# Kernel optimization log

Measured on AMD Instinct MI355X. Metric: run time of the kernel, lower is better.

## Reference

```python
import jax, jax.numpy as jnp
import numpy as np


def _layernorm(x, g, b, eps=1e-5):
    mu = x.mean(-1, keepdims=True)
    var = ((x - mu) ** 2).mean(-1, keepdims=True)
    return (x - mu) / jnp.sqrt(var + eps) * g + b


def _bilinear_sample(feat, coords):
    # feat: (B,C,H,W,D); coords: (B,C,N,2) normalized to [-1,1]
    # torch.grid_sample(mode='bilinear', padding_mode='zeros', align_corners=True)
    B, C, H, W, D = feat.shape
    x = (coords[..., 0] + 1.0) * 0.5 * (W - 1)  # grid x -> width axis
    y = (coords[..., 1] + 1.0) * 0.5 * (H - 1)  # grid y -> height axis
    x0 = jnp.floor(x)
    y0 = jnp.floor(y)
    wx1 = x - x0
    wy1 = y - y0
    bi = jnp.arange(B)[:, None, None]
    ci = jnp.arange(C)[None, :, None]

    def corner(yi, xi, w):
        inb = (xi >= 0) & (xi < W) & (yi >= 0) & (yi < H)
        xc = jnp.clip(xi, 0, W - 1).astype(jnp.int32)
        yc = jnp.clip(yi, 0, H - 1).astype(jnp.int32)
        v = feat[bi, ci, yc, xc]  # (B,C,N,D) gather
        return v * (w * inb)[..., None]

    return (corner(y0, x0, (1 - wy1) * (1 - wx1))
            + corner(y0, x0 + 1, (1 - wy1) * wx1)
            + corner(y0 + 1, x0, wy1 * (1 - wx1))
            + corner(y0 + 1, x0 + 1, wy1 * wx1))


def setup_inputs() -> dict:
    key = jax.random.key(0)
    ks = jax.random.split(key, 12)
    B, C, N, D, H, W = 2, 8, 16384, 256, 64, 64
    s = 1.0 / np.sqrt(D).astype(np.float32)
    return {
        "queries": jax.random.normal(ks[0], (B, N, D), jnp.float32),
        "image_features": jax.random.normal(ks[1], (B, C, H, W, D), jnp.float32),
        "pixel_coords": jax.random.uniform(ks[2], (B, C, N, 2), jnp.float32) * 2.0 - 1.0,
        "valid_mask": jax.random.randint(ks[3], (B, C, N), 0, 2).astype(jnp.int32),
        "Wq": jax.random.normal(ks[4], (D, D), jnp.float32) * s,
        "bq": jnp.zeros((D,), jnp.float32),
        "Wkv": jax.random.normal(ks[5], (D, 2 * D), jnp.float32) * s,
        "bkv": jnp.zeros((2 * D,), jnp.float32),
        "Wo": jax.random.normal(ks[6], (D, D), jnp.float32) * s,
        "bo": jnp.zeros((D,), jnp.float32),
        "gamma": jnp.ones((D,), jnp.float32),
        "beta": jnp.zeros((D,), jnp.float32),
    }


def reference(queries, image_features, pixel_coords, valid_mask,
              Wq, bq, Wkv, bkv, Wo, bo, gamma, beta):
    B, N, D = queries.shape
    residual = queries
    qn = _layernorm(queries, gamma, beta)
    sampled = _bilinear_sample(image_features, pixel_coords)      # (B,C,N,D)
    sampled = jnp.transpose(sampled, (0, 2, 1, 3))                 # (B,N,C,D)
    q = qn @ Wq + bq                                               # (B,N,D)
    kv = sampled @ Wkv + bkv                                       # (B,N,C,2D)
    k, v = kv[..., :D], kv[..., D:]
    scores = jnp.einsum('bnd,bncd->bnc', q, k) / jnp.sqrt(jnp.float32(D))
    valid = jnp.transpose(valid_mask, (0, 2, 1)) != 0              # (B,N,C)
    scores = jnp.where(valid, scores, -jnp.inf)
    attn = jax.nn.softmax(scores, axis=-1)
    attn = jnp.where(jnp.isnan(attn), 0.0, attn)                   # all-invalid -> 0
    out = jnp.einsum('bnc,bncd->bnd', attn, v)
    return residual + out @ Wo + bo
```

## Files before the change

### kernel.cpp

```cpp
#include <hip/hip_runtime.h>
#include <math.h>

#define NROWS 32768

typedef __attribute__((ext_vector_type(8))) short short8;
typedef __attribute__((ext_vector_type(4))) float f32x4;

#define WS_ABF    0
#define WS_WVOBF  32768
#define WS_PB     65536
#define WS_BVO    65792
#define WS_FEATBF 8487424

__device__ __forceinline__ unsigned short f2bf(float f) {
    unsigned u = __builtin_bit_cast(unsigned, f);
    u += 0x7FFFu + ((u >> 16) & 1u);
    return (unsigned short)(u >> 16);
}
__device__ __forceinline__ float bf_lo(unsigned u) {
    return __builtin_bit_cast(float, u << 16);
}
__device__ __forceinline__ float bf_hi(unsigned u) {
    return __builtin_bit_cast(float, u & 0xFFFF0000u);
}

__global__ __launch_bounds__(256)
void precompute_kernel(const float* __restrict__ Wq, const float* __restrict__ bq,
                       const float* __restrict__ Wkv, const float* __restrict__ bkv,
                       const float* __restrict__ Wo, const float* __restrict__ feat,
                       float* __restrict__ ws) {
    int t = threadIdx.x;
    int blk = blockIdx.x;
    if (blk >= 514) {
        long i = (long)(blk - 514) * 1024 + t * 4;
        float4 v = *(const float4*)(feat + i);
        unsigned lo = (unsigned)f2bf(v.x) | ((unsigned)f2bf(v.y) << 16);
        unsigned hi = (unsigned)f2bf(v.z) | ((unsigned)f2bf(v.w) << 16);
        *(uint2*)((unsigned short*)(ws + WS_FEATBF) + i) = make_uint2(lo, hi);
        return;
    }
    if (blk < 256) {
        int f = blk;
        const float4* wq4 = (const float4*)(Wq + f * 256);
        const float4* wk4 = (const float4*)(Wkv + (long)t * 512);
        float acc = 0.f;
        #pragma unroll 8
        for (int d4 = 0; d4 < 64; ++d4) {
            float4 a = wq4[d4], b = wk4[d4];
            acc += a.x * b.x + a.y * b.y + a.z * b.z + a.w * b.w;
        }
        ((unsigned short*)(ws + WS_ABF))[t * 256 + f] = f2bf(acc);
    } else if (blk < 512) {
        int e = blk - 256;
        float acc = 0.f;
        for (int g = 0; g < 256; ++g)
            acc = fmaf(Wkv[(long)e * 512 + 256 + g], Wo[g * 256 + t], acc);
        ((unsigned short*)(ws + WS_WVOBF))[t * 256 + e] = f2bf(acc);
    } else if (blk == 512) {
        float acc = 0.f;
        for (int d = 0; d < 256; ++d)
            acc = fmaf(bq[d], Wkv[(long)t * 512 + d], acc);
        ws[WS_PB + t] = acc;
    } else {
        float acc = 0.f;
        for (int g = 0; g < 256; ++g)
            acc = fmaf(bkv[256 + g], Wo[g * 256 + t], acc);
        ws[WS_BVO + t] = acc;
    }
}

#define RPB  32
#define SLOT 260

__global__ __launch_bounds__(256, 4)
void fused_rowpipe(const float* __restrict__ queries, const float* __restrict__ gamma,
                   const float* __restrict__ beta, const float* __restrict__ coords,
                   const int* __restrict__ vmask, const float* __restrict__ bo,
                   const float* __restrict__ ws, float* __restrict__ out) {
    __shared__ float buf[RPB * SLOT + RPB];
    float* ssu = buf + RPB * SLOT;

    const unsigned short* Abf    = (const unsigned short*)(ws + WS_ABF);
    const unsigned short* Wvobf  = (const unsigned short*)(ws + WS_WVOBF);
    const float*          pb     = ws + WS_PB;
    const float*          bvo    = ws + WS_BVO;
    const unsigned short* featbf = (const unsigned short*)(ws + WS_FEATBF);

    int tid = threadIdx.x, wave = tid >> 6, lane = tid & 63;
    long row0 = (long)blockIdx.x * RPB;

    {
        float4 g4 = *(const float4*)(gamma + 4 * lane);
        float4 b4 = *(const float4*)(beta + 4 * lane);
        #pragma unroll
        for (int rr = 0; rr < 8; ++rr) {
            int r = wave * 8 + rr;
            float4 v = *(const float4*)(queries + (row0 + r) * 256 + 4 * lane);
            float s = v.x + v.y + v.z + v.w;
            s += __shfl_xor(s, 32); s += __shfl_xor(s, 16); s += __shfl_xor(s, 8);
            s += __shfl_xor(s, 4);  s += __shfl_xor(s, 2);  s += __shfl_xor(s, 1);
            float mu = s * 0.00390625f;
            float dx = v.x - mu, dy = v.y - mu, dz = v.z - mu, dw = v.w - mu;
            float vv = dx * dx + dy * dy + dz * dz + dw * dw;
            vv += __shfl_xor(vv, 32); vv += __shfl_xor(vv, 16); vv += __shfl_xor(vv, 8);
            vv += __shfl_xor(vv, 4);  vv += __shfl_xor(vv, 2);  vv += __shfl_xor(vv, 1);
            float rstd = rsqrtf(vv * 0.00390625f + 1e-5f);
            float qx = dx * rstd * g4.x + b4.x;
            float qy = dy * rstd * g4.y + b4.y;
            float qz = dz * rstd * g4.z + b4.z;
            float qw = dw * rstd * g4.w + b4.w;
            unsigned lo = (unsigned)f2bf(qx) | ((unsigned)f2bf(qy) << 16);
            unsigned hi = (unsigned)f2bf(qz) | ((unsigned)f2bf(qw) << 16);
            *(uint2*)((unsigned short*)&buf[r * SLOT] + 4 * lane) = make_uint2(lo, hi);
        }
    }
    __syncthreads();

    int r16 = lane & 15, g = lane >> 4;
    f32x4 zero = {0.f, 0.f, 0.f, 0.f};

    {
        f32x4 acc[2][4];
        #pragma unroll
        for (int mt = 0; mt < 2; ++mt)
            #pragma unroll
            for (int nt = 0; nt < 4; ++nt) acc[mt][nt] = zero;

        #pragma unroll
        for (int ks = 0; ks < 8; ++ks) {
            short8 bfr[4], afr[2];
            #pragma unroll
            for (int nt = 0; nt < 4; ++nt)
                bfr[nt] = *(const short8*)(Abf + ((wave * 64 + nt * 16 + r16) << 8) + ks * 32 + g * 8);
            #pragma unroll
            for (int mt = 0; mt < 2; ++mt)
                afr[mt] = *(const short8*)((const unsigned short*)buf + (mt * 16 + r16) * (SLOT * 2) + ks * 32 + g * 8);
            #pragma unroll
            for (int mt = 0; mt < 2; ++mt)
                #pragma unroll
                for (int nt = 0; nt < 4; ++nt)
                    acc[mt][nt] = __builtin_amdgcn_mfma_f32_16x16x32_bf16(afr[mt], bfr[nt], acc[mt][nt], 0, 0, 0);
        }
        __syncthreads();

        float pbv[4];
        #pragma unroll
        for (int nt = 0; nt < 4; ++nt) pbv[nt] = pb[wave * 64 + nt * 16 + r16];
        #pragma unroll
        for (int mt = 0; mt < 2; ++mt)
            #pragma unroll
            for (int nt = 0; nt < 4; ++nt)
                #pragma unroll
                for (int rg = 0; rg < 4; ++rg)
                    buf[(mt * 16 + g * 4 + rg) * SLOT + wave * 64 + nt * 16 + r16] =
                        acc[mt][nt][rg] + pbv[nt];
    }
    __syncthreads();

    for (int rr = 0; rr < 8; ++rr) {
        int r = wave * 8 + rr;
        int rowu = __builtin_amdgcn_readfirstlane((int)(row0 + r));
        int b = rowu >> 14;
        int n = rowu & 16383;

        float4 p4 = *(const float4*)(&buf[r * SLOT + 4 * lane]);

        float4 sc[8];
        float score[8];
        bool vld[8];
        #pragma unroll
        for (int c = 0; c < 8; ++c) {
            long cb = (long)(b * 8 + c) * 16384 + n;
            float cx = coords[2 * cb];
            float cy = coords[2 * cb + 1];
            vld[c] = (vmask[cb] != 0);
            float x = (cx + 1.f) * 31.5f;
            float y = (cy + 1.f) * 31.5f;
            float x0f = floorf(x), y0f = floorf(y);
            float wx = x - x0f, wy = y - y0f;
            int ix0 = (int)x0f, iy0 = (int)y0f;
            int ix1 = ix0 + 1, iy1 = iy0 + 1;
            float bx0 = (ix0 >= 0 && ix0 < 64) ? 1.f : 0.f;
            float bx1 = (ix1 >= 0 && ix1 < 64) ? 1.f : 0.f;
            float by0 = (iy0 >= 0 && iy0 < 64) ? 1.f : 0.f;
            float by1 = (iy1 >= 0 && iy1 < 64) ? 1.f : 0.f;
            int cx0 = min(max(ix0, 0), 63), cx1 = min(max(ix1, 0), 63);
            int cy0 = min(max(iy0, 0), 63), cy1 = min(max(iy1, 0), 63);
            const unsigned short* fb = featbf + ((long)(b * 8 + c) << 20);
            const uint2* r00 = (const uint2*)(fb + ((cy0 * 64 + cx0) << 8)) + lane;
            const uint2* r01 = (const uint2*)(fb + ((cy0 * 64 + cx1) << 8)) + lane;
            const uint2* r10 = (const uint2*)(fb + ((cy1 * 64 + cx0) << 8)) + lane;
            const uint2* r11 = (const uint2*)(fb + ((cy1 * 64 + cx1) << 8)) + lane;
            float w00 = (1.f - wy) * (1.f - wx) * by0 * bx0;
            float w01 = (1.f - wy) * wx * by0 * bx1;
            float w10 = wy * (1.f - wx) * by1 * bx0;
            float w11 = wy * wx * by1 * bx1;
            uint2 v00 = *r00, v01 = *r01, v10 = *r10, v11 = *r11;
            float4 s;
            s.x = w00 * bf_lo(v00.x) + w01 * bf_lo(v01.x) + w10 * bf_lo(v10.x) + w11 * bf_lo(v11.x);
            s.y = w00 * bf_hi(v00.x) + w01 * bf_hi(v01.x) + w10 * bf_hi(v10.x) + w11 * bf_hi(v11.x);
            s.z = w00 * bf_lo(v00.y) + w01 * bf_lo(v01.y) + w10 * bf_lo(v10.y) + w11 * bf_lo(v11.y);
            s.w = w00 * bf_hi(v00.y) + w01 * bf_hi(v01.y) + w10 * bf_hi(v10.y) + w11 * bf_hi(v11.y);
            sc[c] = s;
            float t = s.x * p4.x + s.y * p4.y + s.z * p4.z + s.w * p4.w;
            t += __shfl_xor(t, 32); t += __shfl_xor(t, 16); t += __shfl_xor(t, 8);
            t += __shfl_xor(t, 4);  t += __shfl_xor(t, 2);  t += __shfl_xor(t, 1);
            score[c] = t * 0.0625f;
        }

        float m = -INFINITY;
        #pragma unroll
        for (int c = 0; c < 8; ++c) if (vld[c]) m = fmaxf(m, score[c]);
        float4 sb = {0.f, 0.f, 0.f, 0.f};
        float sa = 0.f;
        if (m > -INFINITY) {
            float w[8], s = 0.f;
            #pragma unroll
            for (int c = 0; c < 8; ++c) { w[c] = vld[c] ? __expf(score[c] - m) : 0.f; s += w[c]; }
            float inv = 1.f / s;
            #pragma unroll
            for (int c = 0; c < 8; ++c) {
                float a = w[c] * inv;
                sb.x = fmaf(a, sc[c].x, sb.x);
                sb.y = fmaf(a, sc[c].y, sb.y);
                sb.z = fmaf(a, sc[c].z, sb.z);
                sb.w = fmaf(a, sc[c].w, sb.w);
            }
            sa = 1.f;
        }
        unsigned lo = (unsigned)f2bf(sb.x) | ((unsigned)f2bf(sb.y) << 16);
        unsigned hi = (unsigned)f2bf(sb.z) | ((unsigned)f2bf(sb.w) << 16);
        *(uint2*)((unsigned short*)&buf[r * SLOT] + 4 * lane) = make_uint2(lo, hi);
        if (lane == 0) ssu[r] = sa;
    }
    __syncthreads();

    {
        f32x4 acc2[2][4];
        #pragma unroll
        for (int mt = 0; mt < 2; ++mt)
            #pragma unroll
            for (int nt = 0; nt < 4; ++nt) acc2[mt][nt] = zero;

        #pragma unroll
        for (int ks = 0; ks < 8; ++ks) {
            short8 bfr[4], afr[2];
            #pragma unroll
            for (int nt = 0; nt < 4; ++nt)
                bfr[nt] = *(const short8*)(Wvobf + ((wave * 64 + nt * 16 + r16) << 8) + ks * 32 + g * 8);
            #pragma unroll
            for (int mt = 0; mt < 2; ++mt)
                afr[mt] = *(const short8*)((const unsigned short*)buf + (mt * 16 + r16) * (SLOT * 2) + ks * 32 + g * 8);
            #pragma unroll
            for (int mt = 0; mt < 2; ++mt)
                #pragma unroll
                for (int nt = 0; nt < 4; ++nt)
                    acc2[mt][nt] = __builtin_amdgcn_mfma_f32_16x16x32_bf16(afr[mt], bfr[nt], acc2[mt][nt], 0, 0, 0);
        }
        __syncthreads();

        #pragma unroll
        for (int mt = 0; mt < 2; ++mt)
            #pragma unroll
            for (int nt = 0; nt < 4; ++nt)
                #pragma unroll
                for (int rg = 0; rg < 4; ++rg)
                    buf[(mt * 16 + g * 4 + rg) * SLOT + wave * 64 + nt * 16 + r16] = acc2[mt][nt][rg];
    }
    __syncthreads();

    {
        float4 bvo4 = *(const float4*)(bvo + 4 * lane);
        float4 bo4  = *(const float4*)(bo + 4 * lane);
        #pragma unroll
        for (int rr = 0; rr < 8; ++rr) {
            int r = wave * 8 + rr;
            float4 q4 = *(const float4*)(queries + (row0 + r) * 256 + 4 * lane);
            float4 a4 = *(const float4*)(&buf[r * SLOT + 4 * lane]);
            float su = ssu[r];
            float4 o;
            o.x = q4.x + a4.x + su * bvo4.x + bo4.x;
            o.y = q4.y + a4.y + su * bvo4.y + bo4.y;
            o.z = q4.z + a4.z + su * bvo4.z + bo4.z;
            o.w = q4.w + a4.w + su * bvo4.w + bo4.w;
            *(float4*)(out + (row0 + r) * 256 + 4 * lane) = o;
        }
    }
}

extern "C" void kernel_launch(void* const* d_in, const int* in_sizes, int n_in,
                              void* d_out, int out_size, void* d_ws, size_t ws_size,
                              hipStream_t stream) {
    const float* queries = (const float*)d_in[0];
    const float* feat    = (const float*)d_in[1];
    const float* coords  = (const float*)d_in[2];
    const int*   vmask   = (const int*)  d_in[3];
    const float* Wq      = (const float*)d_in[4];
    const float* bq      = (const float*)d_in[5];
    const float* Wkv     = (const float*)d_in[6];
    const float* bkv     = (const float*)d_in[7];
    const float* Wo      = (const float*)d_in[8];
    const float* bo      = (const float*)d_in[9];
    const float* gamma   = (const float*)d_in[10];
    const float* beta    = (const float*)d_in[11];
    float* out = (float*)d_out;
    float* ws  = (float*)d_ws;

    precompute_kernel<<<514 + 16384, 256, 0, stream>>>(Wq, bq, Wkv, bkv, Wo, feat, ws);
    fused_rowpipe<<<NROWS / RPB, 256, 0, stream>>>(queries, gamma, beta, coords, vmask, bo, ws, out);
}
```

Baseline: 259.4 us.

## Halve rows per block, use online softmax, stash queries in registers

Cuts rows per block from 32 to 16, so each wave runs one MFMA row tile and the grid has twice as many blocks. The eight-camera softmax becomes an online (running max/sum) accumulation, so the per-camera sampled vectors and scores no longer sit in registers. The residual query values are kept in registers instead of being reloaded from global memory, and the small precompute loops get unroll pragmas. In exchange, each block reloads the weight fragments over half as many rows, and the online softmax adds extra exp calls and rescaling work.

```diff
diff --git a/kernel.cpp b/kernel.cpp
--- a/kernel.cpp
+++ b/kernel.cpp
@@ -53,23 +53,26 @@
     } else if (blk < 512) {
         int e = blk - 256;
         float acc = 0.f;
+        #pragma unroll 8
         for (int g = 0; g < 256; ++g)
             acc = fmaf(Wkv[(long)e * 512 + 256 + g], Wo[g * 256 + t], acc);
         ((unsigned short*)(ws + WS_WVOBF))[t * 256 + e] = f2bf(acc);
     } else if (blk == 512) {
         float acc = 0.f;
+        #pragma unroll 8
         for (int d = 0; d < 256; ++d)
             acc = fmaf(bq[d], Wkv[(long)t * 512 + d], acc);
         ws[WS_PB + t] = acc;
     } else {
         float acc = 0.f;
+        #pragma unroll 8
         for (int g = 0; g < 256; ++g)
             acc = fmaf(bkv[256 + g], Wo[g * 256 + t], acc);
         ws[WS_BVO + t] = acc;
     }
 }
 
-#define RPB  32
+#define RPB  16
 #define SLOT 260
 
 __global__ __launch_bounds__(256, 4)
@@ -89,13 +92,16 @@
     int tid = threadIdx.x, wave = tid >> 6, lane = tid & 63;
     long row0 = (long)blockIdx.x * RPB;
 
+    float4 qstash[4];
+
     {
         float4 g4 = *(const float4*)(gamma + 4 * lane);
         float4 b4 = *(const float4*)(beta + 4 * lane);
         #pragma unroll
-        for (int rr = 0; rr < 8; ++rr) {
-            int r = wave * 8 + rr;
+        for (int rr = 0; rr < 4; ++rr) {
+            int r = wave * 4 + rr;
             float4 v = *(const float4*)(queries + (row0 + r) * 256 + 4 * lane);
+            qstash[rr] = v;
             float s = v.x + v.y + v.z + v.w;
             s += __shfl_xor(s, 32); s += __shfl_xor(s, 16); s += __shfl_xor(s, 8);
             s += __shfl_xor(s, 4);  s += __shfl_xor(s, 2);  s += __shfl_xor(s, 1);
@@ -120,26 +126,20 @@
     f32x4 zero = {0.f, 0.f, 0.f, 0.f};
 
     {
-        f32x4 acc[2][4];
-        #pragma unroll
-        for (int mt = 0; mt < 2; ++mt)
-            #pragma unroll
-            for (int nt = 0; nt < 4; ++nt) acc[mt][nt] = zero;
+        f32x4 acc[4];
+        #pragma unroll
+        for (int nt = 0; nt < 4; ++nt) acc[nt] = zero;
 
         #pragma unroll
         for (int ks = 0; ks < 8; ++ks) {
-            short8 bfr[4], afr[2];
+            short8 bfr[4], afr;
             #pragma unroll
             for (int nt = 0; nt < 4; ++nt)
                 bfr[nt] = *(const short8*)(Abf + ((wave * 64 + nt * 16 + r16) << 8) + ks * 32 + g * 8);
-            #pragma unroll
-            for (int mt = 0; mt < 2; ++mt)
-                afr[mt] = *(const short8*)((const unsigned short*)buf + (mt * 16 + r16) * (SLOT * 2) + ks * 32 + g * 8);
-            #pragma unroll
-            for (int mt = 0; mt < 2; ++mt)
-                #pragma unroll
-                for (int nt = 0; nt < 4; ++nt)
-                    acc[mt][nt] = __builtin_amdgcn_mfma_f32_16x16x32_bf16(afr[mt], bfr[nt], acc[mt][nt], 0, 0, 0);
+            afr = *(const short8*)((const unsigned short*)buf + r16 * (SLOT * 2) + ks * 32 + g * 8);
+            #pragma unroll
+            for (int nt = 0; nt < 4; ++nt)
+                acc[nt] = __builtin_amdgcn_mfma_f32_16x16x32_bf16(afr, bfr[nt], acc[nt], 0, 0, 0);
         }
         __syncthreads();
 
@@ -147,33 +147,30 @@
         #pragma unroll
         for (int nt = 0; nt < 4; ++nt) pbv[nt] = pb[wave * 64 + nt * 16 + r16];
         #pragma unroll
-        for (int mt = 0; mt < 2; ++mt)
-            #pragma unroll
-            for (int nt = 0; nt < 4; ++nt)
-                #pragma unroll
-                for (int rg = 0; rg < 4; ++rg)
-                    buf[(mt * 16 + g * 4 + rg) * SLOT + wave * 64 + nt * 16 + r16] =
-                        acc[mt][nt][rg] + pbv[nt];
+        for (int nt = 0; nt < 4; ++nt)
+            #pragma unroll
+            for (int rg = 0; rg < 4; ++rg)
+                buf[(g * 4 + rg) * SLOT + wave * 64 + nt * 16 + r16] = acc[nt][rg] + pbv[nt];
     }
     __syncthreads();
 
-    for (int rr = 0; rr < 8; ++rr) {
-        int r = wave * 8 + rr;
+    for (int rr = 0; rr < 4; ++rr) {
+        int r = wave * 4 + rr;
         int rowu = __builtin_amdgcn_readfirstlane((int)(row0 + r));
         int b = rowu >> 14;
         int n = rowu & 16383;
 
         float4 p4 = *(const float4*)(&buf[r * SLOT + 4 * lane]);
 
-        float4 sc[8];
-        float score[8];
-        bool vld[8];
+        float m = -INFINITY, ssum = 0.f;
+        float4 sbacc = {0.f, 0.f, 0.f, 0.f};
+
         #pragma unroll
         for (int c = 0; c < 8; ++c) {
             long cb = (long)(b * 8 + c) * 16384 + n;
             float cx = coords[2 * cb];
             float cy = coords[2 * cb + 1];
-            vld[c] = (vmask[cb] != 0);
+            bool vld = (vmask[cb] != 0);
             float x = (cx + 1.f) * 31.5f;
             float y = (cy + 1.f) * 31.5f;
             float x0f = floorf(x), y0f = floorf(y);
@@ -201,31 +198,31 @@
             s.y = w00 * bf_hi(v00.x) + w01 * bf_hi(v01.x) + w10 * bf_hi(v10.x) + w11 * bf_hi(v11.x);
             s.z = w00 * bf_lo(v00.y) + w01 * bf_lo(v01.y) + w10 * bf_lo(v10.y) + w11 * bf_lo(v11.y);
             s.w = w00 * bf_hi(v00.y) + w01 * bf_hi(v01.y) + w10 * bf_hi(v10.y) + w11 * bf_hi(v11.y);
-            sc[c] = s;
             float t = s.x * p4.x + s.y * p4.y + s.z * p4.z + s.w * p4.w;
             t += __shfl_xor(t, 32); t += __shfl_xor(t, 16); t += __shfl_xor(t, 8);
             t += __shfl_xor(t, 4);  t += __shfl_xor(t, 2);  t += __shfl_xor(t, 1);
-            score[c] = t * 0.0625f;
-        }
-
-        float m = -INFINITY;
-        #pragma unroll
-        for (int c = 0; c < 8; ++c) if (vld[c]) m = fmaxf(m, score[c]);
+            t *= 0.0625f;
+            if (vld) {
+                float nm = fmaxf(m, t);
+                float scale = __expf(m - nm);
+                float w = __expf(t - nm);
+                ssum = ssum * scale + w;
+                sbacc.x = fmaf(w, s.x, sbacc.x * scale);
+                sbacc.y = fmaf(w, s.y, sbacc.y * scale);
+                sbacc.z = fmaf(w, s.z, sbacc.z * scale);
+                sbacc.w = fmaf(w, s.w, sbacc.w * scale);
+                m = nm;
+            }
+        }
+
         float4 sb = {0.f, 0.f, 0.f, 0.f};
         float sa = 0.f;
         if (m > -INFINITY) {
-            float w[8], s = 0.f;
-            #pragma unroll
-            for (int c = 0; c < 8; ++c) { w[c] = vld[c] ? __expf(score[c] - m) : 0.f; s += w[c]; }
-            float inv = 1.f / s;
-            #pragma unroll
-            for (int c = 0; c < 8; ++c) {
-                float a = w[c] * inv;
-                sb.x = fmaf(a, sc[c].x, sb.x);
-                sb.y = fmaf(a, sc[c].y, sb.y);
-                sb.z = fmaf(a, sc[c].z, sb.z);
-                sb.w = fmaf(a, sc[c].w, sb.w);
-            }
+            float inv = 1.f / ssum;
+            sb.x = sbacc.x * inv;
+            sb.y = sbacc.y * inv;
+            sb.z = sbacc.z * inv;
+            sb.w = sbacc.w * inv;
             sa = 1.f;
         }
         unsigned lo = (unsigned)f2bf(sb.x) | ((unsigned)f2bf(sb.y) << 16);
@@ -236,36 +233,28 @@
     __syncthreads();
 
     {
-        f32x4 acc2[2][4];
-        #pragma unroll
-        for (int mt = 0; mt < 2; ++mt)
-            #pragma unroll
-            for (int nt = 0; nt < 4; ++nt) acc2[mt][nt] = zero;
+        f32x4 acc2[4];
+        #pragma unroll
+        for (int nt = 0; nt < 4; ++nt) acc2[nt] = zero;
 
         #pragma unroll
         for (int ks = 0; ks < 8; ++ks) {
-            short8 bfr[4], afr[2];
+            short8 bfr[4], afr;
             #pragma unroll
             for (int nt = 0; nt < 4; ++nt)
                 bfr[nt] = *(const short8*)(Wvobf + ((wave * 64 + nt * 16 + r16) << 8) + ks * 32 + g * 8);
-            #pragma unroll
-            for (int mt = 0; mt < 2; ++mt)
-                afr[mt] = *(const short8*)((const unsigned short*)buf + (mt * 16 + r16) * (SLOT * 2) + ks * 32 + g * 8);
-            #pragma unroll
-            for (int mt = 0; mt < 2; ++mt)
-                #pragma unroll
-                for (int nt = 0; nt < 4; ++nt)
-                    acc2[mt][nt] = __builtin_amdgcn_mfma_f32_16x16x32_bf16(afr[mt], bfr[nt], acc2[mt][nt], 0, 0, 0);
+            afr = *(const short8*)((const unsigned short*)buf + r16 * (SLOT * 2) + ks * 32 + g * 8);
+            #pragma unroll
+            for (int nt = 0; nt < 4; ++nt)
+                acc2[nt] = __builtin_amdgcn_mfma_f32_16x16x32_bf16(afr, bfr[nt], acc2[nt], 0, 0, 0);
         }
         __syncthreads();
 
         #pragma unroll
-        for (int mt = 0; mt < 2; ++mt)
-            #pragma unroll
-            for (int nt = 0; nt < 4; ++nt)
-                #pragma unroll
-                for (int rg = 0; rg < 4; ++rg)
-                    buf[(mt * 16 + g * 4 + rg) * SLOT + wave * 64 + nt * 16 + r16] = acc2[mt][nt][rg];
+        for (int nt = 0; nt < 4; ++nt)
+            #pragma unroll
+            for (int rg = 0; rg < 4; ++rg)
+                buf[(g * 4 + rg) * SLOT + wave * 64 + nt * 16 + r16] = acc2[nt][rg];
     }
     __syncthreads();
 
@@ -273,9 +262,9 @@
         float4 bvo4 = *(const float4*)(bvo + 4 * lane);
         float4 bo4  = *(const float4*)(bo + 4 * lane);
         #pragma unroll
-        for (int rr = 0; rr < 8; ++rr) {
-            int r = wave * 8 + rr;
-            float4 q4 = *(const float4*)(queries + (row0 + r) * 256 + 4 * lane);
+        for (int rr = 0; rr < 4; ++rr) {
+            int r = wave * 4 + rr;
+            float4 q4 = qstash[rr];
             float4 a4 = *(const float4*)(&buf[r * SLOT + 4 * lane]);
             float su = ssu[r];
             float4 o;
```

Measured after the change: 287.7 us. 10.9% more time.
